# Kernel optimization log

Hardware: AMD Instinct MI355X
Metric: run time of the kernel (lower is better)

Reference implementation:

```python
import jax, jax.numpy as jnp
import numpy as np

N = 50000
E = 800000
D_IN, D_HID, D_OUT = 128, 128, 64


def setup_inputs() -> dict:
    key = jax.random.key(0)
    ks = jax.random.split(key, 8)
    x = jax.random.normal(ks[0], (N, D_IN), dtype=jnp.float32)
    edge_index = jax.random.randint(ks[1], (2, E), 0, N, dtype=jnp.int64)
    # Glorot-ish init for GCNConv linear weights + zero bias (PyG default bias=True)
    def lin(k, din, dout):
        s = 1.0 / np.sqrt(din)
        return jax.random.uniform(k, (din, dout), jnp.float32, -s, s)
    return {
        "x": x,
        "edge_index": edge_index,
        "W1": lin(ks[2], D_IN, D_HID), "b1": jnp.zeros((D_HID,), jnp.float32),
        "W2": lin(ks[3], D_HID, D_HID), "b2": jnp.zeros((D_HID,), jnp.float32),
        "W3": lin(ks[4], D_HID, D_OUT), "b3": jnp.zeros((D_OUT,), jnp.float32),
    }


def _prep_edges(edge_index, n):
    # add self loops (PyG GCNConv default add_self_loops=True)
    loop = jnp.arange(n, dtype=edge_index.dtype)
    src = jnp.concatenate([edge_index[0], loop])
    dst = jnp.concatenate([edge_index[1], loop])
    deg = jax.ops.segment_sum(jnp.ones_like(dst, dtype=jnp.float32), dst, num_segments=n)
    dinv = jnp.where(deg > 0, jax.lax.rsqrt(deg), 0.0)
    norm = dinv[src] * dinv[dst]  # symmetric normalization per edge
    return src, dst, norm


def _gcn_conv(h, W, b, src, dst, norm, n):
    h = h @ W                                   # [N, dout]
    msg = h[src] * norm[:, None]                # [E+N, dout] gather
    out = jax.ops.segment_sum(msg, dst, num_segments=n)  # scatter-add
    return out + b


def reference(x, edge_index, W1, b1, W2, b2, W3, b3):
    src, dst, norm = _prep_edges(edge_index, N)
    h = jax.nn.relu(_gcn_conv(x, W1, b1, src, dst, norm, N))
    h = jax.nn.relu(_gcn_conv(h, W2, b2, src, dst, norm, N))
    return _gcn_conv(h, W3, b3, src, dst, norm, N)  # eval mode: dropout is identity
```

## Files before the change

### kernel.cpp

```cpp
#include <hip/hip_runtime.h>
#include <hip/hip_fp16.h>
#include <math.h>

#define NN 50000
#define NE 800000
#define RAWSTRIDE 96
#define NBUCK 196
#define NBBIN 196
#define BCAP 4608
#define ACH 4096
#define G1B 782

using bf8v = __attribute__((ext_vector_type(8))) short;
using f4v  = __attribute__((ext_vector_type(4))) float;

__device__ inline unsigned short f2bf(float f) {
    unsigned int u = __float_as_uint(f);
    u += 0x7FFFu + ((u >> 16) & 1u);
    return (unsigned short)(u >> 16);
}
__device__ inline float bflo(unsigned int d) { return __uint_as_float(d << 16); }
__device__ inline float bfhi(unsigned int d) { return __uint_as_float(d & 0xFFFF0000u); }


__device__ __forceinline__ void bin_body(const int* __restrict__ src,
                                         const int* __restrict__ dst,
                                         int* __restrict__ gcursor,
                                         unsigned int* __restrict__ bst,
                                         int bx, char* shc) {
    unsigned int* items = (unsigned int*)shc;
    int* cnt    = (int*)(shc + 16384);
    int* pref   = (int*)(shc + 17408);
    int* gstart = (int*)(shc + 18436);
    const int t = threadIdx.x;
    cnt[t] = 0;
    __syncthreads();
    const int base = bx * ACH;

    unsigned int my[16]; int myb[16], myr[16];
    #pragma unroll
    for (int i = 0; i < 16; ++i) {
        int e = base + i * 256 + t;
        my[i] = 0; myb[i] = -1; myr[i] = 0;
        if (e < NE) {
            int d = dst[e], s = src[e];
            my[i] = (unsigned int)s | ((unsigned int)d << 16);
            int b = d >> 8;
            myb[i] = b;
            myr[i] = atomicAdd(&cnt[b], 1);
        }
    }
    __syncthreads();
    if (t == 0) {
        int run = 0;
        for (int b = 0; b < 256; ++b) { pref[b] = run; run += cnt[b]; }
        pref[256] = run;
    }
    __syncthreads();
    if (cnt[t] > 0) gstart[t] = atomicAdd(&gcursor[t], cnt[t]);
    __syncthreads();
    #pragma unroll
    for (int i = 0; i < 16; ++i)
        if (myb[i] >= 0) items[pref[myb[i]] + myr[i]] = my[i];
    __syncthreads();
    const int total = pref[256];
    for (int i = t; i < total; i += 256) {
        int lo = 0, hi = 255;
        while (lo < hi) { int mid = (lo + hi + 1) >> 1; if (pref[mid] <= i) lo = mid; else hi = mid - 1; }
        int idx = gstart[lo] + (i - pref[lo]);
        if (idx < BCAP) bst[(size_t)lo * BCAP + idx] = items[i];
    }
}


__global__ __launch_bounds__(512) void sortb_kernel(const int* __restrict__ gcursor,
                                                    const unsigned int* __restrict__ bst,
                                                    int* __restrict__ cnt_g,
                                                    float* __restrict__ dinv,
                                                    unsigned short* __restrict__ raw) {
    __shared__ unsigned int items[BCAP];
    __shared__ int cnt[256], pref[257], cur[256];
    __shared__ unsigned short outl[BCAP];
    const int b = blockIdx.x;
    const int t = threadIdx.x;
    int n = gcursor[b];
    if (n > BCAP) n = BCAP;
    if (t < 256) { cnt[t] = 0; cur[t] = 0; }
    __syncthreads();
    for (int i = t; i < n; i += 512) {
        unsigned int u = bst[(size_t)b * BCAP + i];
        items[i] = u;
        atomicAdd(&cnt[(u >> 16) & 255], 1);
    }
    __syncthreads();
    if (t == 0) {
        int run = 0;
        for (int j = 0; j < 256; ++j) { pref[j] = run; run += cnt[j]; }
        pref[256] = run;
    }
    __syncthreads();
    for (int i = t; i < n; i += 512) {
        unsigned int u = items[i];
        int ln = (u >> 16) & 255;
        int r = atomicAdd(&cur[ln], 1);
        outl[pref[ln] + r] = (unsigned short)(u & 0xFFFFu);
    }
    __syncthreads();
    for (int i = t; i < n; i += 512) {
        int lo = 0, hi = 255;
        while (lo < hi) { int mid = (lo + hi + 1) >> 1; if (pref[mid] <= i) lo = mid; else hi = mid - 1; }
        int r = i - pref[lo];
        if (r < RAWSTRIDE) raw[(size_t)(b * 256 + lo) * RAWSTRIDE + r] = outl[i];
    }
    if (t < 256) {
        int node = b * 256 + t;
        if (node < NN) {
            int c = cnt[t];
            cnt_g[node] = c;
            dinv[node] = rsqrtf((float)(1 + c));
        }
    }
}


template <bool A_FP32>
__device__ __forceinline__ void gemm128_body(const void* __restrict__ Ain,
                                             const float* __restrict__ W,
                                             unsigned short* __restrict__ out,
                                             int bx, char* shc) {
    unsigned short* Wt = (unsigned short*)shc;
    unsigned short* Dt = (unsigned short*)(shc + 128 * 136 * 2);
    const int t = threadIdx.x;
    const int row0 = bx * 64;

    {
        int n = t & 127;
        int kbase = (t >> 7) * 4;
        for (int kk = kbase; kk < 128; kk += 8) {
            float w0 = W[(kk + 0) * 128 + n];
            float w1 = W[(kk + 1) * 128 + n];
            float w2 = W[(kk + 2) * 128 + n];
            float w3 = W[(kk + 3) * 128 + n];
            unsigned int p0 = (unsigned int)f2bf(w0) | ((unsigned int)f2bf(w1) << 16);
            unsigned int p1 = (unsigned int)f2bf(w2) | ((unsigned int)f2bf(w3) << 16);
            *(unsigned int*)&Wt[n * 136 + kk]     = p0;
            *(unsigned int*)&Wt[n * 136 + kk + 2] = p1;
        }
    }
    __syncthreads();

    const int wave = t >> 6;
    const int lane = t & 63;
    const int m16  = lane & 15;
    const int quad = lane >> 4;
    const int arow = row0 + wave * 16 + m16;
    const int arowc = (arow < NN) ? arow : 0;

    f4v acc[8];
    #pragma unroll
    for (int i = 0; i < 8; ++i) acc[i] = (f4v)(0.0f);

    #pragma unroll
    for (int k0 = 0; k0 < 128; k0 += 32) {
        bf8v afrag;
        if (A_FP32) {
            const float* A = (const float*)Ain;
            const float4* ap = (const float4*)(A + (size_t)arowc * 128 + k0 + quad * 8);
            float4 a0 = ap[0], a1 = ap[1];
            afrag[0] = (short)f2bf(a0.x); afrag[1] = (short)f2bf(a0.y);
            afrag[2] = (short)f2bf(a0.z); afrag[3] = (short)f2bf(a0.w);
            afrag[4] = (short)f2bf(a1.x); afrag[5] = (short)f2bf(a1.y);
            afrag[6] = (short)f2bf(a1.z); afrag[7] = (short)f2bf(a1.w);
        } else {
            const unsigned short* A = (const unsigned short*)Ain;
            afrag = *(const bf8v*)(A + (size_t)arowc * 128 + k0 + quad * 8);
        }
        #pragma unroll
        for (int nt = 0; nt < 8; ++nt) {
            bf8v bfrag = *(const bf8v*)&Wt[(nt * 16 + m16) * 136 + k0 + quad * 8];
            acc[nt] = __builtin_amdgcn_mfma_f32_16x16x32_bf16(afrag, bfrag, acc[nt], 0, 0, 0);
        }
    }

    #pragma unroll
    for (int nt = 0; nt < 8; ++nt) {
        #pragma unroll
        for (int r = 0; r < 4; ++r) {
            Dt[(wave * 16 + quad * 4 + r) * 136 + nt * 16 + m16] = f2bf(acc[nt][r]);
        }
    }
    __syncthreads();

    {
        int r = t >> 2;
        int c = t & 3;
        int gr = row0 + r;
        if (gr < NN) {
            const uint4* s = (const uint4*)&Dt[r * 136] + c * 4;
            uint4* d = (uint4*)(out + (size_t)gr * 128) + c * 4;
            d[0] = s[0]; d[1] = s[1]; d[2] = s[2]; d[3] = s[3];
        }
    }
}

__global__ __launch_bounds__(256) void bin_g1_kernel(const int* __restrict__ src,
                                                     const int* __restrict__ dst,
                                                     int* __restrict__ gcursor,
                                                     unsigned int* __restrict__ bst,
                                                     const float* __restrict__ x,
                                                     const float* __restrict__ W1,
                                                     unsigned short* __restrict__ hb) {
    __shared__ __align__(16) char sh[52224];
    if (blockIdx.x < NBBIN) {
        bin_body(src, dst, gcursor, bst, blockIdx.x, sh);
    } else {
        gemm128_body<true>(x, W1, hb, blockIdx.x - NBBIN, sh);
    }
}

__global__ __launch_bounds__(256) void mfma_gemm_kernel(const unsigned short* __restrict__ Ain,
                                                        const float* __restrict__ W,
                                                        unsigned short* __restrict__ out) {
    __shared__ __align__(16) char sh[52224];
    gemm128_body<false>(Ain, W, out, blockIdx.x, sh);
}


template <bool RELU>
__global__ __launch_bounds__(256) void agg_bf16_kernel(const unsigned short* __restrict__ hin,
                                                       const unsigned short* __restrict__ raw,
                                                       const int* __restrict__ cnt_g,
                                                       const float* __restrict__ dinv,
                                                       const float* __restrict__ bias,
                                                       unsigned short* __restrict__ outb) {
    const int t = threadIdx.x;
    const int group = t >> 4;
    const int lane  = t & 15;
    const int wid = blockIdx.x * 16 + group;
    if (wid >= NN) return;

    int c = cnt_g[wid];
    if (c > RAWSTRIDE) c = RAWSTRIDE;
    const float diw = dinv[wid];
    const unsigned short* rrow = raw + (size_t)wid * RAWSTRIDE;
    const uint4* hv = (const uint4*)hin;

    float acc[8];
    {
        uint4 g = hv[(size_t)wid * 16 + lane];
        float ws = diw * diw;
        acc[0] = ws * bflo(g.x); acc[1] = ws * bfhi(g.x);
        acc[2] = ws * bflo(g.y); acc[3] = ws * bfhi(g.y);
        acc[4] = ws * bflo(g.z); acc[5] = ws * bfhi(g.z);
        acc[6] = ws * bflo(g.w); acc[7] = ws * bfhi(g.w);
    }

    #define ACCUM(G, W_) \
        acc[0] += W_ * bflo(G.x); acc[1] += W_ * bfhi(G.x); \
        acc[2] += W_ * bflo(G.y); acc[3] += W_ * bfhi(G.y); \
        acc[4] += W_ * bflo(G.z); acc[5] += W_ * bfhi(G.z); \
        acc[6] += W_ * bflo(G.w); acc[7] += W_ * bfhi(G.w);

    const int cfull = c & ~7;
    for (int e = 0; e < cfull; e += 8) {
        uint4 q = *(const uint4*)(rrow + e);
        int c0 = q.x & 0xFFFFu, c1 = q.x >> 16;
        int c2 = q.y & 0xFFFFu, c3 = q.y >> 16;
        int c4 = q.z & 0xFFFFu, c5 = q.z >> 16;
        int c6 = q.w & 0xFFFFu, c7 = q.w >> 16;
        float w0 = diw * dinv[c0], w1 = diw * dinv[c1];
        float w2 = diw * dinv[c2], w3 = diw * dinv[c3];
        float w4 = diw * dinv[c4], w5 = diw * dinv[c5];
        float w6 = diw * dinv[c6], w7 = diw * dinv[c7];
        uint4 g0 = hv[(size_t)c0 * 16 + lane];
        uint4 g1 = hv[(size_t)c1 * 16 + lane];
        uint4 g2 = hv[(size_t)c2 * 16 + lane];
        uint4 g3 = hv[(size_t)c3 * 16 + lane];
        uint4 g4 = hv[(size_t)c4 * 16 + lane];
        uint4 g5 = hv[(size_t)c5 * 16 + lane];
        uint4 g6 = hv[(size_t)c6 * 16 + lane];
        uint4 g7 = hv[(size_t)c7 * 16 + lane];
        ACCUM(g0, w0) ACCUM(g1, w1) ACCUM(g2, w2) ACCUM(g3, w3)
        ACCUM(g4, w4) ACCUM(g5, w5) ACCUM(g6, w6) ACCUM(g7, w7)
    }
    if (c & 7) {
        int e = cfull, rem = c - e;
        uint4 q = *(const uint4*)(rrow + e);
        int c0 = q.x & 0xFFFFu, c1 = q.x >> 16;
        int c2 = q.y & 0xFFFFu, c3 = q.y >> 16;
        int c4 = q.z & 0xFFFFu, c5 = q.z >> 16;
        int c6 = q.w & 0xFFFFu, c7 = q.w >> 16;
        if (rem <= 1) c1 = 0; if (rem <= 2) c2 = 0; if (rem <= 3) c3 = 0;
        if (rem <= 4) c4 = 0; if (rem <= 5) c5 = 0; if (rem <= 6) c6 = 0;
        c7 = (rem <= 7) ? 0 : c7;
        float w0 = diw * dinv[c0];
        float w1 = (rem > 1) ? diw * dinv[c1] : 0.f;
        float w2 = (rem > 2) ? diw * dinv[c2] : 0.f;
        float w3 = (rem > 3) ? diw * dinv[c3] : 0.f;
        float w4 = (rem > 4) ? diw * dinv[c4] : 0.f;
        float w5 = (rem > 5) ? diw * dinv[c5] : 0.f;
        float w6 = (rem > 6) ? diw * dinv[c6] : 0.f;
        float w7 = 0.f;
        uint4 g0 = hv[(size_t)c0 * 16 + lane];
        uint4 g1 = hv[(size_t)c1 * 16 + lane];
        uint4 g2 = hv[(size_t)c2 * 16 + lane];
        uint4 g3 = hv[(size_t)c3 * 16 + lane];
        uint4 g4 = hv[(size_t)c4 * 16 + lane];
        uint4 g5 = hv[(size_t)c5 * 16 + lane];
        uint4 g6 = hv[(size_t)c6 * 16 + lane];
        uint4 g7 = hv[(size_t)c7 * 16 + lane];
        ACCUM(g0, w0) ACCUM(g1, w1) ACCUM(g2, w2) ACCUM(g3, w3)
        ACCUM(g4, w4) ACCUM(g5, w5) ACCUM(g6, w6) ACCUM(g7, w7)
    }
    #undef ACCUM

    const float4* bp = (const float4*)bias;
    float4 b0 = bp[lane * 2], b1 = bp[lane * 2 + 1];
    acc[0] += b0.x; acc[1] += b0.y; acc[2] += b0.z; acc[3] += b0.w;
    acc[4] += b1.x; acc[5] += b1.y; acc[6] += b1.z; acc[7] += b1.w;
    if (RELU) {
        #pragma unroll
        for (int j = 0; j < 8; ++j) acc[j] = fmaxf(acc[j], 0.f);
    }
    uint4 o;
    o.x = (unsigned int)f2bf(acc[0]) | ((unsigned int)f2bf(acc[1]) << 16);
    o.y = (unsigned int)f2bf(acc[2]) | ((unsigned int)f2bf(acc[3]) << 16);
    o.z = (unsigned int)f2bf(acc[4]) | ((unsigned int)f2bf(acc[5]) << 16);
    o.w = (unsigned int)f2bf(acc[6]) | ((unsigned int)f2bf(acc[7]) << 16);
    ((uint4*)(outb + (size_t)wid * 128))[lane] = o;
}


__global__ __launch_bounds__(256) void gemm3_kernel(const unsigned short* __restrict__ Ab,
                                                    const float* __restrict__ W,
                                                    unsigned short* __restrict__ outh) {
    constexpr int CG = 16;
    constexpr int RPT = 4;
    constexpr int ROWS = 64;
    constexpr int LD = 132;
    __shared__ float lds[ROWS * LD];
    const int t = threadIdx.x;
    const int row0 = blockIdx.x * ROWS;

    #pragma unroll
    for (int j = 0; j < ROWS / 8; ++j) {
        int idx4 = j * 256 + t;
        int r = idx4 >> 5, c4 = idx4 & 31;
        int gr = row0 + r;
        uint2 u = make_uint2(0u, 0u);
        if (gr < NN) u = ((const uint2*)(Ab + (size_t)gr * 128))[c4];
        float4 v;
        v.x = bflo(u.x); v.y = bfhi(u.x); v.z = bflo(u.y); v.w = bfhi(u.y);
        ((float4*)(lds + r * LD))[c4] = v;
    }
    __syncthreads();

    const int cg = t % CG;
    const int rt = t / CG;
    const float4* Wv = (const float4*)W;
    float4 acc[RPT];
    #pragma unroll
    for (int i = 0; i < RPT; ++i) acc[i] = make_float4(0.f, 0.f, 0.f, 0.f);

    for (int k0 = 0; k0 < 128; k0 += 4) {
        float4 w0 = Wv[(k0 + 0) * CG + cg];
        float4 w1 = Wv[(k0 + 1) * CG + cg];
        float4 w2 = Wv[(k0 + 2) * CG + cg];
        float4 w3 = Wv[(k0 + 3) * CG + cg];
        #pragma unroll
        for (int i = 0; i < RPT; ++i) {
            const float* lr = lds + (rt * RPT + i) * LD;
            float4 a = ((const float4*)lr)[k0 >> 2];
            acc[i].x += a.x * w0.x + a.y * w1.x + a.z * w2.x + a.w * w3.x;
            acc[i].y += a.x * w0.y + a.y * w1.y + a.z * w2.y + a.w * w3.y;
            acc[i].z += a.x * w0.z + a.y * w1.z + a.z * w2.z + a.w * w3.z;
            acc[i].w += a.x * w0.w + a.y * w1.w + a.z * w2.w + a.w * w3.w;
        }
    }

    #pragma unroll
    for (int i = 0; i < RPT; ++i) {
        int gr = row0 + rt * RPT + i;
        if (gr < NN) {
            uint2 o;
            o.x = (unsigned int)f2bf(acc[i].x) | ((unsigned int)f2bf(acc[i].y) << 16);
            o.y = (unsigned int)f2bf(acc[i].z) | ((unsigned int)f2bf(acc[i].w) << 16);
            ((uint2*)(outh + (size_t)gr * 64))[cg] = o;
        }
    }
}


__global__ __launch_bounds__(256) void agg3_kernel(const unsigned short* __restrict__ hin,
                                                   const unsigned short* __restrict__ raw,
                                                   const int* __restrict__ cnt_g,
                                                   const float* __restrict__ dinv,
                                                   const float* __restrict__ bias,
                                                   float* __restrict__ out) {
    const int t = threadIdx.x;
    const int group = t >> 3;
    const int lane  = t & 7;
    const int wid = blockIdx.x * 32 + group;
    if (wid >= NN) return;

    int c = cnt_g[wid];
    if (c > RAWSTRIDE) c = RAWSTRIDE;
    const float diw = dinv[wid];
    const unsigned short* rrow = raw + (size_t)wid * RAWSTRIDE;
    const uint4* hv = (const uint4*)hin;

    float acc[8];
    {
        uint4 g = hv[(size_t)wid * 8 + lane];
        float ws = diw * diw;
        acc[0] = ws * bflo(g.x); acc[1] = ws * bfhi(g.x);
        acc[2] = ws * bflo(g.y); acc[3] = ws * bfhi(g.y);
        acc[4] = ws * bflo(g.z); acc[5] = ws * bfhi(g.z);
        acc[6] = ws * bflo(g.w); acc[7] = ws * bfhi(g.w);
    }

    #define ACCUM(G, W_) \
        acc[0] += W_ * bflo(G.x); acc[1] += W_ * bfhi(G.x); \
        acc[2] += W_ * bflo(G.y); acc[3] += W_ * bfhi(G.y); \
        acc[4] += W_ * bflo(G.z); acc[5] += W_ * bfhi(G.z); \
        acc[6] += W_ * bflo(G.w); acc[7] += W_ * bfhi(G.w);

    const int cfull = c & ~7;
    for (int e = 0; e < cfull; e += 8) {
        uint4 q = *(const uint4*)(rrow + e);
        int c0 = q.x & 0xFFFFu, c1 = q.x >> 16;
        int c2 = q.y & 0xFFFFu, c3 = q.y >> 16;
        int c4 = q.z & 0xFFFFu, c5 = q.z >> 16;
        int c6 = q.w & 0xFFFFu, c7 = q.w >> 16;
        float w0 = diw * dinv[c0], w1 = diw * dinv[c1];
        float w2 = diw * dinv[c2], w3 = diw * dinv[c3];
        float w4 = diw * dinv[c4], w5 = diw * dinv[c5];
        float w6 = diw * dinv[c6], w7 = diw * dinv[c7];
        uint4 g0 = hv[(size_t)c0 * 8 + lane];
        uint4 g1 = hv[(size_t)c1 * 8 + lane];
        uint4 g2 = hv[(size_t)c2 * 8 + lane];
        uint4 g3 = hv[(size_t)c3 * 8 + lane];
        uint4 g4 = hv[(size_t)c4 * 8 + lane];
        uint4 g5 = hv[(size_t)c5 * 8 + lane];
        uint4 g6 = hv[(size_t)c6 * 8 + lane];
        uint4 g7 = hv[(size_t)c7 * 8 + lane];
        ACCUM(g0, w0) ACCUM(g1, w1) ACCUM(g2, w2) ACCUM(g3, w3)
        ACCUM(g4, w4) ACCUM(g5, w5) ACCUM(g6, w6) ACCUM(g7, w7)
    }
    if (c & 7) {
        int e = cfull, rem = c - e;
        uint4 q = *(const uint4*)(rrow + e);
        int c0 = q.x & 0xFFFFu, c1 = q.x >> 16;
        int c2 = q.y & 0xFFFFu, c3 = q.y >> 16;
        int c4 = q.z & 0xFFFFu, c5 = q.z >> 16;
        int c6 = q.w & 0xFFFFu, c7 = q.w >> 16;
        if (rem <= 1) c1 = 0; if (rem <= 2) c2 = 0; if (rem <= 3) c3 = 0;
        if (rem <= 4) c4 = 0; if (rem <= 5) c5 = 0; if (rem <= 6) c6 = 0;
        c7 = (rem <= 7) ? 0 : c7;
        float w0 = diw * dinv[c0];
        float w1 = (rem > 1) ? diw * dinv[c1] : 0.f;
        float w2 = (rem > 2) ? diw * dinv[c2] : 0.f;
        float w3 = (rem > 3) ? diw * dinv[c3] : 0.f;
        float w4 = (rem > 4) ? diw * dinv[c4] : 0.f;
        float w5 = (rem > 5) ? diw * dinv[c5] : 0.f;
        float w6 = (rem > 6) ? diw * dinv[c6] : 0.f;
        float w7 = 0.f;
        uint4 g0 = hv[(size_t)c0 * 8 + lane];
        uint4 g1 = hv[(size_t)c1 * 8 + lane];
        uint4 g2 = hv[(size_t)c2 * 8 + lane];
        uint4 g3 = hv[(size_t)c3 * 8 + lane];
        uint4 g4 = hv[(size_t)c4 * 8 + lane];
        uint4 g5 = hv[(size_t)c5 * 8 + lane];
        uint4 g6 = hv[(size_t)c6 * 8 + lane];
        uint4 g7 = hv[(size_t)c7 * 8 + lane];
        ACCUM(g0, w0) ACCUM(g1, w1) ACCUM(g2, w2) ACCUM(g3, w3)
        ACCUM(g4, w4) ACCUM(g5, w5) ACCUM(g6, w6) ACCUM(g7, w7)
    }
    #undef ACCUM

    const float4* bp = (const float4*)bias;
    float4 b0 = bp[lane * 2], b1 = bp[lane * 2 + 1];
    acc[0] += b0.x; acc[1] += b0.y; acc[2] += b0.z; acc[3] += b0.w;
    acc[4] += b1.x; acc[5] += b1.y; acc[6] += b1.z; acc[7] += b1.w;

    float4 o0 = make_float4(acc[0], acc[1], acc[2], acc[3]);
    float4 o1 = make_float4(acc[4], acc[5], acc[6], acc[7]);
    ((float4*)(out + (size_t)wid * 64))[lane * 2]     = o0;
    ((float4*)(out + (size_t)wid * 64))[lane * 2 + 1] = o1;
}


extern "C" void kernel_launch(void* const* d_in, const int* in_sizes, int n_in,
                              void* d_out, int out_size, void* d_ws, size_t ws_size,
                              hipStream_t stream) {
    const float* x  = (const float*)d_in[0];
    const int*   ei = (const int*)d_in[1];
    const float* W1 = (const float*)d_in[2];
    const float* b1 = (const float*)d_in[3];
    const float* W2 = (const float*)d_in[4];
    const float* b2 = (const float*)d_in[5];
    const float* W3 = (const float*)d_in[6];
    const float* b3 = (const float*)d_in[7];
    float* out = (float*)d_out;

    char* w = (char*)d_ws;
    int*   cnt_g   = (int*)  (w + 0x0000000);
    int*   gcursor = (int*)  (w + 0x0040000);
    float* dinv    = (float*)(w + 0x0048000);
    unsigned int*   bst = (unsigned int*)  (w + 0x0080000);
    unsigned short* raw = (unsigned short*)(w + 0x0400000);
    unsigned short* hb  = (unsigned short*)(w + 0x0E00000);
    unsigned short* zb  = (unsigned short*)(w + 0x1B00000);
    unsigned short* h3b = (unsigned short*)(w + 0x2800000);

    const int* src = ei;
    const int* dst = ei + NE;

    hipMemsetAsync(gcursor, 0, NBUCK * sizeof(int), stream);
    bin_g1_kernel<<<NBBIN + G1B, 256, 0, stream>>>(src, dst, gcursor, bst, x, W1, hb);
    sortb_kernel<<<NBUCK, 512, 0, stream>>>(gcursor, bst, cnt_g, dinv, raw);
    agg_bf16_kernel<true><<<(NN + 15) / 16, 256, 0, stream>>>(hb, raw, cnt_g, dinv, b1, zb);
    mfma_gemm_kernel<<<G1B, 256, 0, stream>>>(zb, W2, hb);
    agg_bf16_kernel<true><<<(NN + 15) / 16, 256, 0, stream>>>(hb, raw, cnt_g, dinv, b2, zb);
    gemm3_kernel<<<G1B, 256, 0, stream>>>(zb, W3, h3b);
    agg3_kernel<<<(NN + 31) / 32, 256, 0, stream>>>(h3b, raw, cnt_g, dinv, b3, out);
}
```

Before: 244.8 us.

## Replace two-pass bucket sort CSR build with direct atomic scatter into padded rows

The two-stage binning plus per-bucket sort that built padded adjacency rows is replaced by a single scatter in which each edge does a global atomicAdd on its destination count and writes its source into a fixed-stride row. This drops one kernel launch, the intermediate bucket buffer and the dinv array. Degree normalisation is now recomputed with rsqrtf from the counts inside the aggregation kernels. In exchange, neighbour order within a row becomes nondeterministic, so floating-point summation order can vary between runs, and the scatter relies on many global atomics with scattered 2-byte writes.

```diff
diff --git a/kernel.cpp b/kernel.cpp
--- a/kernel.cpp
+++ b/kernel.cpp
@@ -5,10 +5,7 @@
 #define NN 50000
 #define NE 800000
 #define RAWSTRIDE 96
-#define NBUCK 196
-#define NBBIN 196
-#define BCAP 4608
-#define ACH 4096
+#define SB 782
 #define G1B 782
 
 using bf8v = __attribute__((ext_vector_type(8))) short;
@@ -21,106 +18,6 @@
 }
 __device__ inline float bflo(unsigned int d) { return __uint_as_float(d << 16); }
 __device__ inline float bfhi(unsigned int d) { return __uint_as_float(d & 0xFFFF0000u); }
-
-
-__device__ __forceinline__ void bin_body(const int* __restrict__ src,
-                                         const int* __restrict__ dst,
-                                         int* __restrict__ gcursor,
-                                         unsigned int* __restrict__ bst,
-                                         int bx, char* shc) {
-    unsigned int* items = (unsigned int*)shc;
-    int* cnt    = (int*)(shc + 16384);
-    int* pref   = (int*)(shc + 17408);
-    int* gstart = (int*)(shc + 18436);
-    const int t = threadIdx.x;
-    cnt[t] = 0;
-    __syncthreads();
-    const int base = bx * ACH;
-
-    unsigned int my[16]; int myb[16], myr[16];
-    #pragma unroll
-    for (int i = 0; i < 16; ++i) {
-        int e = base + i * 256 + t;
-        my[i] = 0; myb[i] = -1; myr[i] = 0;
-        if (e < NE) {
-            int d = dst[e], s = src[e];
-            my[i] = (unsigned int)s | ((unsigned int)d << 16);
-            int b = d >> 8;
-            myb[i] = b;
-            myr[i] = atomicAdd(&cnt[b], 1);
-        }
-    }
-    __syncthreads();
-    if (t == 0) {
-        int run = 0;
-        for (int b = 0; b < 256; ++b) { pref[b] = run; run += cnt[b]; }
-        pref[256] = run;
-    }
-    __syncthreads();
-    if (cnt[t] > 0) gstart[t] = atomicAdd(&gcursor[t], cnt[t]);
-    __syncthreads();
-    #pragma unroll
-    for (int i = 0; i < 16; ++i)
-        if (myb[i] >= 0) items[pref[myb[i]] + myr[i]] = my[i];
-    __syncthreads();
-    const int total = pref[256];
-    for (int i = t; i < total; i += 256) {
-        int lo = 0, hi = 255;
-        while (lo < hi) { int mid = (lo + hi + 1) >> 1; if (pref[mid] <= i) lo = mid; else hi = mid - 1; }
-        int idx = gstart[lo] + (i - pref[lo]);
-        if (idx < BCAP) bst[(size_t)lo * BCAP + idx] = items[i];
-    }
-}
-
-
-__global__ __launch_bounds__(512) void sortb_kernel(const int* __restrict__ gcursor,
-                                                    const unsigned int* __restrict__ bst,
-                                                    int* __restrict__ cnt_g,
-                                                    float* __restrict__ dinv,
-                                                    unsigned short* __restrict__ raw) {
-    __shared__ unsigned int items[BCAP];
-    __shared__ int cnt[256], pref[257], cur[256];
-    __shared__ unsigned short outl[BCAP];
-    const int b = blockIdx.x;
-    const int t = threadIdx.x;
-    int n = gcursor[b];
-    if (n > BCAP) n = BCAP;
-    if (t < 256) { cnt[t] = 0; cur[t] = 0; }
-    __syncthreads();
-    for (int i = t; i < n; i += 512) {
-        unsigned int u = bst[(size_t)b * BCAP + i];
-        items[i] = u;
-        atomicAdd(&cnt[(u >> 16) & 255], 1);
-    }
-    __syncthreads();
-    if (t == 0) {
-        int run = 0;
-        for (int j = 0; j < 256; ++j) { pref[j] = run; run += cnt[j]; }
-        pref[256] = run;
-    }
-    __syncthreads();
-    for (int i = t; i < n; i += 512) {
-        unsigned int u = items[i];
-        int ln = (u >> 16) & 255;
-        int r = atomicAdd(&cur[ln], 1);
-        outl[pref[ln] + r] = (unsigned short)(u & 0xFFFFu);
-    }
-    __syncthreads();
-    for (int i = t; i < n; i += 512) {
-        int lo = 0, hi = 255;
-        while (lo < hi) { int mid = (lo + hi + 1) >> 1; if (pref[mid] <= i) lo = mid; else hi = mid - 1; }
-        int r = i - pref[lo];
-        if (r < RAWSTRIDE) raw[(size_t)(b * 256 + lo) * RAWSTRIDE + r] = outl[i];
-    }
-    if (t < 256) {
-        int node = b * 256 + t;
-        if (node < NN) {
-            int c = cnt[t];
-            cnt_g[node] = c;
-            dinv[node] = rsqrtf((float)(1 + c));
-        }
-    }
-}
 
 
 template <bool A_FP32>
@@ -203,18 +100,33 @@
     }
 }
 
-__global__ __launch_bounds__(256) void bin_g1_kernel(const int* __restrict__ src,
-                                                     const int* __restrict__ dst,
-                                                     int* __restrict__ gcursor,
-                                                     unsigned int* __restrict__ bst,
-                                                     const float* __restrict__ x,
-                                                     const float* __restrict__ W1,
-                                                     unsigned short* __restrict__ hb) {
+
+__global__ __launch_bounds__(256) void scat_g1_kernel(const int* __restrict__ src,
+                                                      const int* __restrict__ dst,
+                                                      int* __restrict__ cnt_g,
+                                                      unsigned short* __restrict__ raw,
+                                                      const float* __restrict__ x,
+                                                      const float* __restrict__ W1,
+                                                      unsigned short* __restrict__ hb) {
     __shared__ __align__(16) char sh[52224];
-    if (blockIdx.x < NBBIN) {
-        bin_body(src, dst, gcursor, bst, blockIdx.x, sh);
+    if (blockIdx.x < SB) {
+        int idx = blockIdx.x * 256 + threadIdx.x;
+        int e0 = idx * 4;
+        if (e0 < NE) {
+            int4 s4 = *(const int4*)(src + e0);
+            int4 d4 = *(const int4*)(dst + e0);
+            int p;
+            p = atomicAdd(cnt_g + d4.x, 1);
+            if (p < RAWSTRIDE) raw[(size_t)d4.x * RAWSTRIDE + p] = (unsigned short)s4.x;
+            p = atomicAdd(cnt_g + d4.y, 1);
+            if (p < RAWSTRIDE) raw[(size_t)d4.y * RAWSTRIDE + p] = (unsigned short)s4.y;
+            p = atomicAdd(cnt_g + d4.z, 1);
+            if (p < RAWSTRIDE) raw[(size_t)d4.z * RAWSTRIDE + p] = (unsigned short)s4.z;
+            p = atomicAdd(cnt_g + d4.w, 1);
+            if (p < RAWSTRIDE) raw[(size_t)d4.w * RAWSTRIDE + p] = (unsigned short)s4.w;
+        }
     } else {
-        gemm128_body<true>(x, W1, hb, blockIdx.x - NBBIN, sh);
+        gemm128_body<true>(x, W1, hb, blockIdx.x - SB, sh);
     }
 }
 
@@ -230,7 +142,6 @@
 __global__ __launch_bounds__(256) void agg_bf16_kernel(const unsigned short* __restrict__ hin,
                                                        const unsigned short* __restrict__ raw,
                                                        const int* __restrict__ cnt_g,
-                                                       const float* __restrict__ dinv,
                                                        const float* __restrict__ bias,
                                                        unsigned short* __restrict__ outb) {
     const int t = threadIdx.x;
@@ -239,9 +150,9 @@
     const int wid = blockIdx.x * 16 + group;
     if (wid >= NN) return;
 
-    int c = cnt_g[wid];
-    if (c > RAWSTRIDE) c = RAWSTRIDE;
-    const float diw = dinv[wid];
+    const int cn = cnt_g[wid];
+    int c = (cn > RAWSTRIDE) ? RAWSTRIDE : cn;
+    const float diw = rsqrtf(1.0f + (float)cn);
     const unsigned short* rrow = raw + (size_t)wid * RAWSTRIDE;
     const uint4* hv = (const uint4*)hin;
 
@@ -260,6 +171,7 @@
         acc[2] += W_ * bflo(G.y); acc[3] += W_ * bfhi(G.y); \
         acc[4] += W_ * bflo(G.z); acc[5] += W_ * bfhi(G.z); \
         acc[6] += W_ * bflo(G.w); acc[7] += W_ * bfhi(G.w);
+    #define EW(CI) (diw * rsqrtf(1.0f + (float)cnt_g[CI]))
 
     const int cfull = c & ~7;
     for (int e = 0; e < cfull; e += 8) {
@@ -268,10 +180,8 @@
         int c2 = q.y & 0xFFFFu, c3 = q.y >> 16;
         int c4 = q.z & 0xFFFFu, c5 = q.z >> 16;
         int c6 = q.w & 0xFFFFu, c7 = q.w >> 16;
-        float w0 = diw * dinv[c0], w1 = diw * dinv[c1];
-        float w2 = diw * dinv[c2], w3 = diw * dinv[c3];
-        float w4 = diw * dinv[c4], w5 = diw * dinv[c5];
-        float w6 = diw * dinv[c6], w7 = diw * dinv[c7];
+        float w0 = EW(c0), w1 = EW(c1), w2 = EW(c2), w3 = EW(c3);
+        float w4 = EW(c4), w5 = EW(c5), w6 = EW(c6), w7 = EW(c7);
         uint4 g0 = hv[(size_t)c0 * 16 + lane];
         uint4 g1 = hv[(size_t)c1 * 16 + lane];
         uint4 g2 = hv[(size_t)c2 * 16 + lane];
@@ -292,14 +202,14 @@
         int c6 = q.w & 0xFFFFu, c7 = q.w >> 16;
         if (rem <= 1) c1 = 0; if (rem <= 2) c2 = 0; if (rem <= 3) c3 = 0;
         if (rem <= 4) c4 = 0; if (rem <= 5) c5 = 0; if (rem <= 6) c6 = 0;
-        c7 = (rem <= 7) ? 0 : c7;
-        float w0 = diw * dinv[c0];
-        float w1 = (rem > 1) ? diw * dinv[c1] : 0.f;
-        float w2 = (rem > 2) ? diw * dinv[c2] : 0.f;
-        float w3 = (rem > 3) ? diw * dinv[c3] : 0.f;
-        float w4 = (rem > 4) ? diw * dinv[c4] : 0.f;
-        float w5 = (rem > 5) ? diw * dinv[c5] : 0.f;
-        float w6 = (rem > 6) ? diw * dinv[c6] : 0.f;
+        c7 = 0;
+        float w0 = EW(c0);
+        float w1 = (rem > 1) ? EW(c1) : 0.f;
+        float w2 = (rem > 2) ? EW(c2) : 0.f;
+        float w3 = (rem > 3) ? EW(c3) : 0.f;
+        float w4 = (rem > 4) ? EW(c4) : 0.f;
+        float w5 = (rem > 5) ? EW(c5) : 0.f;
+        float w6 = (rem > 6) ? EW(c6) : 0.f;
         float w7 = 0.f;
         uint4 g0 = hv[(size_t)c0 * 16 + lane];
         uint4 g1 = hv[(size_t)c1 * 16 + lane];
@@ -312,6 +222,7 @@
         ACCUM(g0, w0) ACCUM(g1, w1) ACCUM(g2, w2) ACCUM(g3, w3)
         ACCUM(g4, w4) ACCUM(g5, w5) ACCUM(g6, w6) ACCUM(g7, w7)
     }
+    #undef EW
     #undef ACCUM
 
     const float4* bp = (const float4*)bias;
@@ -394,7 +305,6 @@
 __global__ __launch_bounds__(256) void agg3_kernel(const unsigned short* __restrict__ hin,
                                                    const unsigned short* __restrict__ raw,
                                                    const int* __restrict__ cnt_g,
-                                                   const float* __restrict__ dinv,
                                                    const float* __restrict__ bias,
                                                    float* __restrict__ out) {
     const int t = threadIdx.x;
@@ -403,9 +313,9 @@
     const int wid = blockIdx.x * 32 + group;
     if (wid >= NN) return;
 
-    int c = cnt_g[wid];
-    if (c > RAWSTRIDE) c = RAWSTRIDE;
-    const float diw = dinv[wid];
+    const int cn = cnt_g[wid];
+    int c = (cn > RAWSTRIDE) ? RAWSTRIDE : cn;
+    const float diw = rsqrtf(1.0f + (float)cn);
     const unsigned short* rrow = raw + (size_t)wid * RAWSTRIDE;
     const uint4* hv = (const uint4*)hin;
 
@@ -424,6 +334,7 @@
         acc[2] += W_ * bflo(G.y); acc[3] += W_ * bfhi(G.y); \
         acc[4] += W_ * bflo(G.z); acc[5] += W_ * bfhi(G.z); \
         acc[6] += W_ * bflo(G.w); acc[7] += W_ * bfhi(G.w);
+    #define EW(CI) (diw * rsqrtf(1.0f + (float)cnt_g[CI]))
 
     const int cfull = c & ~7;
     for (int e = 0; e < cfull; e += 8) {
@@ -432,10 +343,8 @@
         int c2 = q.y & 0xFFFFu, c3 = q.y >> 16;
         int c4 = q.z & 0xFFFFu, c5 = q.z >> 16;
         int c6 = q.w & 0xFFFFu, c7 = q.w >> 16;
-        float w0 = diw * dinv[c0], w1 = diw * dinv[c1];
-        float w2 = diw * dinv[c2], w3 = diw * dinv[c3];
-        float w4 = diw * dinv[c4], w5 = diw * dinv[c5];
-        float w6 = diw * dinv[c6], w7 = diw * dinv[c7];
+        float w0 = EW(c0), w1 = EW(c1), w2 = EW(c2), w3 = EW(c3);
+        float w4 = EW(c4), w5 = EW(c5), w6 = EW(c6), w7 = EW(c7);
         uint4 g0 = hv[(size_t)c0 * 8 + lane];
         uint4 g1 = hv[(size_t)c1 * 8 + lane];
         uint4 g2 = hv[(size_t)c2 * 8 + lane];
@@ -456,14 +365,14 @@
         int c6 = q.w & 0xFFFFu, c7 = q.w >> 16;
         if (rem <= 1) c1 = 0; if (rem <= 2) c2 = 0; if (rem <= 3) c3 = 0;
         if (rem <= 4) c4 = 0; if (rem <= 5) c5 = 0; if (rem <= 6) c6 = 0;
-        c7 = (rem <= 7) ? 0 : c7;
-        float w0 = diw * dinv[c0];
-        float w1 = (rem > 1) ? diw * dinv[c1] : 0.f;
-        float w2 = (rem > 2) ? diw * dinv[c2] : 0.f;
-        float w3 = (rem > 3) ? diw * dinv[c3] : 0.f;
-        float w4 = (rem > 4) ? diw * dinv[c4] : 0.f;
-        float w5 = (rem > 5) ? diw * dinv[c5] : 0.f;
-        float w6 = (rem > 6) ? diw * dinv[c6] : 0.f;
+        c7 = 0;
+        float w0 = EW(c0);
+        float w1 = (rem > 1) ? EW(c1) : 0.f;
+        float w2 = (rem > 2) ? EW(c2) : 0.f;
+        float w3 = (rem > 3) ? EW(c3) : 0.f;
+        float w4 = (rem > 4) ? EW(c4) : 0.f;
+        float w5 = (rem > 5) ? EW(c5) : 0.f;
+        float w6 = (rem > 6) ? EW(c6) : 0.f;
         float w7 = 0.f;
         uint4 g0 = hv[(size_t)c0 * 8 + lane];
         uint4 g1 = hv[(size_t)c1 * 8 + lane];
@@ -476,6 +385,7 @@
         ACCUM(g0, w0) ACCUM(g1, w1) ACCUM(g2, w2) ACCUM(g3, w3)
         ACCUM(g4, w4) ACCUM(g5, w5) ACCUM(g6, w6) ACCUM(g7, w7)
     }
+    #undef EW
     #undef ACCUM
 
     const float4* bp = (const float4*)bias;
@@ -505,23 +415,19 @@
 
     char* w = (char*)d_ws;
     int*   cnt_g   = (int*)  (w + 0x0000000);
-    int*   gcursor = (int*)  (w + 0x0040000);
-    float* dinv    = (float*)(w + 0x0048000);
-    unsigned int*   bst = (unsigned int*)  (w + 0x0080000);
-    unsigned short* raw = (unsigned short*)(w + 0x0400000);
-    unsigned short* hb  = (unsigned short*)(w + 0x0E00000);
-    unsigned short* zb  = (unsigned short*)(w + 0x1B00000);
-    unsigned short* h3b = (unsigned short*)(w + 0x2800000);
+    unsigned short* raw = (unsigned short*)(w + 0x0040000);
+    unsigned short* hb  = (unsigned short*)(w + 0x0A00000);
+    unsigned short* zb  = (unsigned short*)(w + 0x1700000);
+    unsigned short* h3b = (unsigned short*)(w + 0x2400000);
 
     const int* src = ei;
     const int* dst = ei + NE;
 
-    hipMemsetAsync(gcursor, 0, NBUCK * sizeof(int), stream);
-    bin_g1_kernel<<<NBBIN + G1B, 256, 0, stream>>>(src, dst, gcursor, bst, x, W1, hb);
-    sortb_kernel<<<NBUCK, 512, 0, stream>>>(gcursor, bst, cnt_g, dinv, raw);
-    agg_bf16_kernel<true><<<(NN + 15) / 16, 256, 0, stream>>>(hb, raw, cnt_g, dinv, b1, zb);
+    hipMemsetAsync(cnt_g, 0, NN * sizeof(int), stream);
+    scat_g1_kernel<<<SB + G1B, 256, 0, stream>>>(src, dst, cnt_g, raw, x, W1, hb);
+    agg_bf16_kernel<true><<<(NN + 15) / 16, 256, 0, stream>>>(hb, raw, cnt_g, b1, zb);
     mfma_gemm_kernel<<<G1B, 256, 0, stream>>>(zb, W2, hb);
-    agg_bf16_kernel<true><<<(NN + 15) / 16, 256, 0, stream>>>(hb, raw, cnt_g, dinv, b2, zb);
+    agg_bf16_kernel<true><<<(NN + 15) / 16, 256, 0, stream>>>(hb, raw, cnt_g, b2, zb);
     gemm3_kernel<<<G1B, 256, 0, stream>>>(zb, W3, h3b);
-    agg3_kernel<<<(NN + 31) / 32, 256, 0, stream>>>(h3b, raw, cnt_g, dinv, b3, out);
-}
+    agg3_kernel<<<(NN + 31) / 32, 256, 0, stream>>>(h3b, raw, cnt_g, b3, out);
+}
```

After: 267.3 us. 1.09x slower.
